# Kernel tuning notes

Measured on AMD Instinct MI355X. Metric: run time of the kernel, lower is better.

## Reference

```python
import jax, jax.numpy as jnp
import numpy as np
import math

D_MODEL = 1024
N_HEADS = 16
D_HEAD = 64


def setup_inputs() -> dict:
    key = jax.random.key(0)
    ks = jax.random.split(key, 9)
    B, T = 2, 2048
    s = 1.0 / math.sqrt(D_MODEL)
    return {
        "x": jax.random.normal(ks[0], (B, T, D_MODEL), dtype=jnp.float32),
        "Wq": jax.random.normal(ks[1], (D_MODEL, D_MODEL), dtype=jnp.float32) * s,
        "bq": jnp.zeros((D_MODEL,), dtype=jnp.float32),
        "Wk": jax.random.normal(ks[2], (D_MODEL, D_MODEL), dtype=jnp.float32) * s,
        "bk": jnp.zeros((D_MODEL,), dtype=jnp.float32),
        "Wv": jax.random.normal(ks[3], (D_MODEL, D_MODEL), dtype=jnp.float32) * s,
        "bv": jnp.zeros((D_MODEL,), dtype=jnp.float32),
        "Wo": jax.random.normal(ks[4], (D_MODEL, D_MODEL), dtype=jnp.float32) * s,
        "bo": jnp.zeros((D_MODEL,), dtype=jnp.float32),
    }


def reference(x, Wq, bq, Wk, bk, Wv, bv, Wo, bo):
    B, T, _ = x.shape
    # Linear layers (torch convention: y = x @ W^T + b)
    Q = x @ Wq.T + bq
    K = x @ Wk.T + bk
    V = x @ Wv.T + bv
    # [B, H, T, Dh]
    Q = Q.reshape(B, T, N_HEADS, D_HEAD).transpose(0, 2, 1, 3)
    K = K.reshape(B, T, N_HEADS, D_HEAD).transpose(0, 2, 1, 3)
    V = V.reshape(B, T, N_HEADS, D_HEAD).transpose(0, 2, 1, 3)
    scores = jnp.einsum("bhqd,bhkd->bhqk", Q, K) / math.sqrt(D_HEAD)
    causal_mask = jnp.tril(jnp.ones((T, T), dtype=bool))  # [T, T]
    scores = jnp.where(causal_mask, scores, -jnp.inf)
    attn = jax.nn.softmax(scores, axis=-1)
    out = jnp.einsum("bhqk,bhkd->bhqd", attn, V)
    out = out.transpose(0, 2, 1, 3).reshape(B, T, D_MODEL)
    return out @ Wo.T + bo
```

## Files before the change

### kernel.cpp

```cpp
#include <hip/hip_runtime.h>

typedef unsigned short u16;
typedef __bf16 bf16x8 __attribute__((ext_vector_type(8)));
typedef float f32x4 __attribute__((ext_vector_type(4)));
typedef float f32x16 __attribute__((ext_vector_type(16)));
typedef u16 u16x4 __attribute__((ext_vector_type(4)));
typedef unsigned int uint;

#define DM 1024
#define MROWS 4096
#define TSEQ 2048

static __device__ __forceinline__ u16 f2b(float f) {
  uint u = __builtin_bit_cast(uint, f);
  uint r = (u + 0x7fffu + ((u >> 16) & 1u)) >> 16;
  return (u16)r;
}

static __device__ __forceinline__ uint pkbf(float a, float b) {
  union { __bf16 h[2]; uint u; } x;
  x.h[0] = (__bf16)a; x.h[1] = (__bf16)b;
  return x.u;
}

__global__ __launch_bounds__(256) void cvt_kernel(const float* __restrict__ in,
                                                  u16* __restrict__ out, int n,
                                                  float scale) {
  int i = (blockIdx.x * 256 + threadIdx.x) * 4;
  if (i >= n) return;
  float4 v = *(const float4*)(in + i);
  u16x4 o;
  o.x = f2b(v.x * scale); o.y = f2b(v.y * scale);
  o.z = f2b(v.z * scale); o.w = f2b(v.w * scale);
  *(u16x4*)(out + i) = o;
}

__global__ __launch_bounds__(256) void cvt4_kernel(
    const float* __restrict__ w0, const float* __restrict__ w1,
    const float* __restrict__ w2, const float* __restrict__ w3,
    u16* __restrict__ o0, u16* __restrict__ o1, u16* __restrict__ o2,
    u16* __restrict__ o3, float s0) {
  const int sel = blockIdx.y;
  const float* in = (sel == 0) ? w0 : (sel == 1) ? w1 : (sel == 2) ? w2 : w3;
  u16* out = (sel == 0) ? o0 : (sel == 1) ? o1 : (sel == 2) ? o2 : o3;
  const float scale = (sel == 0) ? s0 : 1.0f;
  int i = (blockIdx.x * 256 + threadIdx.x) * 4;
  float4 v = *(const float4*)(in + i);
  u16x4 o;
  o.x = f2b(v.x * scale); o.y = f2b(v.y * scale);
  o.z = f2b(v.z * scale); o.w = f2b(v.w * scale);
  *(u16x4*)(out + i) = o;
}

#define SWZ(o) ((o) ^ ((((o) >> 7) & 3) << 4))

static __device__ __forceinline__ void gemm_tile(const u16* __restrict__ A,
                                                 const u16* __restrict__ W,
                                                 int row0, int col0,
                                                 char* ldsA, char* ldsB,
                                                 f32x4 (&acc)[4][4]) {
  const int tid = threadIdx.x;
  const int lane = tid & 63, wid = tid >> 6;
  const int wr = wid >> 1, wc = wid & 1;
  const int lg = lane >> 4, lr = lane & 15;

  f32x4 z = {0.f, 0.f, 0.f, 0.f};
#pragma unroll
  for (int m = 0; m < 4; ++m)
#pragma unroll
    for (int n = 0; n < 4; ++n) acc[m][n] = z;

  for (int k0 = 0; k0 < DM; k0 += 32) {
#pragma unroll
    for (int c = 0; c < 2; ++c) {
      int lin = (c * 256 + tid) * 16;
      int p = SWZ(lin);
      int rowl = p >> 6;
      int cb = p & 63;
      const char* ga = (const char*)(A + (size_t)(row0 + rowl) * DM + k0) + cb;
      __builtin_amdgcn_global_load_lds(
          (const __attribute__((address_space(1))) void*)ga,
          (__attribute__((address_space(3))) void*)(ldsA + lin), 16, 0, 0);
      const char* gb = (const char*)(W + (size_t)(col0 + rowl) * DM + k0) + cb;
      __builtin_amdgcn_global_load_lds(
          (const __attribute__((address_space(1))) void*)gb,
          (__attribute__((address_space(3))) void*)(ldsB + lin), 16, 0, 0);
    }
    __syncthreads();

    bf16x8 av[4], bv[4];
#pragma unroll
    for (int m = 0; m < 4; ++m) {
      int bo = (wr * 64 + m * 16 + lr) * 64 + lg * 16;
      av[m] = *(const bf16x8*)(ldsA + SWZ(bo));
    }
#pragma unroll
    for (int n = 0; n < 4; ++n) {
      int bo = (wc * 64 + n * 16 + lr) * 64 + lg * 16;
      bv[n] = *(const bf16x8*)(ldsB + SWZ(bo));
    }
#pragma unroll
    for (int m = 0; m < 4; ++m)
#pragma unroll
      for (int n = 0; n < 4; ++n)
        acc[m][n] = __builtin_amdgcn_mfma_f32_16x16x32_bf16(av[m], bv[n], acc[m][n], 0, 0, 0);
    __syncthreads();
  }
}

__global__ __launch_bounds__(256) void qkv_gemm(
    const u16* __restrict__ xb, const u16* __restrict__ Wqb,
    const u16* __restrict__ Wkb, const u16* __restrict__ Wvb,
    const float* __restrict__ bq, const float* __restrict__ bk,
    const float* __restrict__ bv, u16* __restrict__ Qx, u16* __restrict__ Kx,
    u16* __restrict__ Vx) {
  __shared__ char lds[16384];
  const int seg = blockIdx.x >> 3, nt = blockIdx.x & 7;
  const int row0 = blockIdx.y * 128, col0 = nt * 128;
  const u16* W = (seg == 0) ? Wqb : (seg == 1) ? Wkb : Wvb;
  const float* bias = (seg == 0) ? bq : (seg == 1) ? bk : bv;
  const float bscale = (seg == 0) ? 0.18033688011112042f : 1.0f;

  f32x4 acc[4][4];
  gemm_tile(xb, W, row0, col0, lds, lds + 8192, acc);

  const int tid = threadIdx.x;
  const int lane = tid & 63, wid = tid >> 6;
  const int wr = wid >> 1, wc = wid & 1;
  const int lg = lane >> 4, lr = lane & 15;

  if (seg < 2) {
    u16* out = (seg == 0) ? Qx : Kx;
#pragma unroll
    for (int m = 0; m < 4; ++m)
#pragma unroll
      for (int n = 0; n < 4; ++n) {
        int col = col0 + wc * 64 + n * 16 + lr;
        float b = bias[col] * bscale;
        int h = col >> 6, dh = col & 63;
        int c = dh >> 4, hi2 = (dh >> 3) & 1, j = dh & 7;
#pragma unroll
        for (int r = 0; r < 4; ++r) {
          int row = row0 + wr * 64 + m * 16 + lg * 4 + r;
          int bI = row >> 11, tt = row & 2047;
          int tw = tt >> 5, ln2 = tt & 31;
          size_t idx =
              ((((((size_t)(bI * 16 + h) * 64 + tw) * 4 + c) * 2 + hi2) * 32) +
               ln2) * 8 + j;
          out[idx] = f2b(acc[m][n][r] + b);
        }
      }
  } else {
#pragma unroll
    for (int m = 0; m < 4; ++m)
#pragma unroll
      for (int n = 0; n < 4; ++n) {
        int col = col0 + wc * 64 + n * 16 + lr;
        float b = bias[col];
        int h = col >> 6, d = col & 63;
        int hh = d >> 5, ln2 = d & 31;
        int t = row0 + wr * 64 + m * 16 + lg * 4;
        int bI = t >> 11, tt = t & 2047;
        int kt = tt >> 5, kvi = tt & 31;
        int c = kvi >> 4, rem = kvi & 15;
        int hi2 = (rem >> 2) & 1, jh = (rem >> 3) & 1;
        u16x4 pk;
        pk.x = f2b(acc[m][n][0] + b);
        pk.y = f2b(acc[m][n][1] + b);
        pk.z = f2b(acc[m][n][2] + b);
        pk.w = f2b(acc[m][n][3] + b);
        size_t idx =
            (((((((size_t)(bI * 16 + h) * 64 + kt) * 2 + c) * 2 + hh) * 2 +
               hi2) * 32) + ln2) * 8 + jh * 4;
        *(u16x4*)(Vx + idx) = pk;
      }
  }
}

__global__ __launch_bounds__(256, 4) void attn_kernel(const u16* __restrict__ Qx,
                                                      const u16* __restrict__ Kx,
                                                      const u16* __restrict__ Vx,
                                                      u16* __restrict__ Aout) {
  __shared__ float mrg[2][64][32];
  __shared__ float mml[2][32][2];
  const int tid = threadIdx.x, lane = tid & 63, wid = tid >> 6;
  const int hi = lane >> 5, ln = lane & 31;
  const int id = blockIdx.x + (blockIdx.y << 5);
  const int xcd = id & 7, idx = id >> 3;
  const int bh = xcd * 4 + (idx & 3);
  const int qt = 31 - (idx >> 2);
  const int b = bh >> 4, h = bh & 15;
  const int q0 = qt * 64 + (wid & 1) * 32;
  const int spl = wid >> 1;
  const int ntile = (q0 >> 5) + 1;
  const int half = (ntile + 1) >> 1;
  const int tbeg = spl ? half : 0;
  const int tend = spl ? ntile : half;

  const u16* Qp = Qx + ((size_t)bh * 64 + (q0 >> 5)) * 2048;
  const u16* Kbb = Kx + (size_t)bh * 64 * 2048;
  const u16* Vbb = Vx + (size_t)bh * 64 * 2048;

  bf16x8 qf[4];
#pragma unroll
  for (int c = 0; c < 4; ++c)
    qf[c] = *(const bf16x8*)(Qp + c * 512 + hi * 256 + ln * 8);

  f32x16 Oa, Ob;
#pragma unroll
  for (int r = 0; r < 16; ++r) { Oa[r] = 0.f; Ob[r] = 0.f; }
  float m = -1e30f, l = 0.f;

  bf16x8 kf[4], vf[4];
  auto loadK = [&](int kt) {
    const u16* Kp = Kbb + (size_t)kt * 2048;
#pragma unroll
    for (int c = 0; c < 4; ++c)
      kf[c] = *(const bf16x8*)(Kp + c * 512 + hi * 256 + ln * 8);
  };
  auto loadV = [&](int kt) {
    const u16* Vp = Vbb + (size_t)kt * 2048;
#pragma unroll
    for (int c = 0; c < 2; ++c)
#pragma unroll
      for (int hh = 0; hh < 2; ++hh)
        vf[2 * c + hh] =
            *(const bf16x8*)(Vp + (c * 2 + hh) * 512 + hi * 256 + ln * 8);
  };

  if (tbeg < tend) loadK(tbeg);
  for (int kt = tbeg; kt < tend; ++kt) {
    const int k0 = kt * 32;
    const bool diag = (kt == ntile - 1);
    loadV(kt);
    f32x16 S;
#pragma unroll
    for (int r = 0; r < 16; ++r) S[r] = 0.f;
    __builtin_amdgcn_s_setprio(1);
#pragma unroll
    for (int c = 0; c < 4; ++c)
      S = __builtin_amdgcn_mfma_f32_32x32x16_bf16(kf[c], qf[c], S, 0, 0, 0);
    __builtin_amdgcn_s_setprio(0);
    if (kt + 1 < tend) loadK(kt + 1);
    if (diag) {
      const int q = q0 + ln;
#pragma unroll
      for (int r = 0; r < 16; ++r) {
        int kv = k0 + (r & 3) + 8 * (r >> 2) + 4 * hi;
        if (kv > q) S[r] = -1e30f;
      }
    }
    float m0 = fmaxf(fmaxf(S[0], S[1]), fmaxf(S[2], S[3]));
    float m1 = fmaxf(fmaxf(S[4], S[5]), fmaxf(S[6], S[7]));
    float m2 = fmaxf(fmaxf(S[8], S[9]), fmaxf(S[10], S[11]));
    float m3 = fmaxf(fmaxf(S[12], S[13]), fmaxf(S[14], S[15]));
    float mx = fmaxf(fmaxf(m0, m1), fmaxf(m2, m3));
    mx = fmaxf(mx, __shfl_xor(mx, 32));
    if (!__all(mx - m <= 8.f)) {
      float nm = fmaxf(m, mx);
      float sf = __builtin_amdgcn_exp2f(m - nm);
      m = nm; l *= sf;
#pragma unroll
      for (int r = 0; r < 16; ++r) { Oa[r] *= sf; Ob[r] *= sf; }
    }
#pragma unroll
    for (int r = 0; r < 16; ++r) S[r] = __builtin_amdgcn_exp2f(S[r] - m);
    float ts = ((S[0] + S[1]) + (S[2] + S[3])) + ((S[4] + S[5]) + (S[6] + S[7]));
    ts += ((S[8] + S[9]) + (S[10] + S[11])) + ((S[12] + S[13]) + (S[14] + S[15]));
    ts += __shfl_xor(ts, 32);
    l += ts;
    uint pw[8];
#pragma unroll
    for (int i = 0; i < 8; ++i) pw[i] = pkbf(S[2 * i], S[2 * i + 1]);
    __builtin_amdgcn_s_setprio(1);
#pragma unroll
    for (int c = 0; c < 2; ++c) {
      union { uint w[4]; bf16x8 v; } pf;
      pf.w[0] = pw[4 * c + 0]; pf.w[1] = pw[4 * c + 1];
      pf.w[2] = pw[4 * c + 2]; pf.w[3] = pw[4 * c + 3];
      Oa = __builtin_amdgcn_mfma_f32_32x32x16_bf16(vf[2 * c + 0], pf.v, Oa, 0, 0, 0);
      Ob = __builtin_amdgcn_mfma_f32_32x32x16_bf16(vf[2 * c + 1], pf.v, Ob, 0, 0, 0);
    }
    __builtin_amdgcn_s_setprio(0);
  }

  union uo { f32x16 v; f32x4 q[4]; };
  const int pi = wid & 1;
  char* moc = (char*)&mrg[pi][0][0];
  const int sw8 = lane & 7;
  if (spl) {
    uo ua, ub; ua.v = Oa; ub.v = Ob;
#pragma unroll
    for (int c = 0; c < 4; ++c) {
      *(f32x4*)(moc + lane * 128 + ((c ^ sw8) * 16)) = ua.q[c];
      *(f32x4*)(moc + lane * 128 + (((c + 4) ^ sw8) * 16)) = ub.q[c];
    }
    if (hi == 0) { mml[pi][ln][0] = m; mml[pi][ln][1] = l; }
  }
  __syncthreads();
  if (spl) return;

  f32x4 rb[8];
#pragma unroll
  for (int c = 0; c < 8; ++c)
    rb[c] = *(const f32x4*)(moc + lane * 128 + ((c ^ sw8) * 16));
  float mB = mml[pi][ln][0], lB = mml[pi][ln][1];
  float M = fmaxf(m, mB);
  float eA = __builtin_amdgcn_exp2f(m - M);
  float eB = __builtin_amdgcn_exp2f(mB - M);
  float inv = 1.f / (l * eA + lB * eB);
  eA *= inv; eB *= inv;
  uo ua, ub; ua.v = Oa; ub.v = Ob;
#pragma unroll
  for (int c = 0; c < 4; ++c) {
    ua.q[c] = ua.q[c] * eA + rb[c] * eB;
    ub.q[c] = ub.q[c] * eA + rb[c + 4] * eB;
  }
  Oa = ua.v; Ob = ub.v;

  char* Tc = moc;
#pragma unroll
  for (int i = 0; i < 8; ++i) {
    int d0 = (2 * i & 3) + 8 * ((2 * i) >> 2) + 4 * hi;
    uint wA = pkbf(Oa[2 * i], Oa[2 * i + 1]);
    *(uint*)(Tc + (ln * 128 + ((d0 * 2) ^ ((ln & 7) << 4)))) = wA;
    uint wB = pkbf(Ob[2 * i], Ob[2 * i + 1]);
    *(uint*)(Tc + (ln * 128 + (((d0 + 32) * 2) ^ ((ln & 7) << 4)))) = wB;
  }
  __threadfence_block();
  u16* Ap = Aout + (size_t)b * TSEQ * DM + h * 64 + (size_t)(q0 + ln) * DM;
#pragma unroll
  for (int j = 0; j < 4; ++j) {
    int oct = hi * 4 + j;
    bf16x8 v = *(const bf16x8*)(Tc + (ln * 128 + ((oct * 16) ^ ((ln & 7) << 4))));
    *(bf16x8*)(Ap + oct * 8) = v;
  }
}

__global__ __launch_bounds__(256) void out_gemm(const u16* __restrict__ attn,
                                                const u16* __restrict__ Wob,
                                                const float* __restrict__ bo,
                                                float* __restrict__ out) {
  __shared__ char lds[16384];
  const int row0 = blockIdx.y * 128, col0 = blockIdx.x * 128;
  f32x4 acc[4][4];
  gemm_tile(attn, Wob, row0, col0, lds, lds + 8192, acc);

  const int tid = threadIdx.x;
  const int lane = tid & 63, wid = tid >> 6;
  const int wr = wid >> 1, wc = wid & 1;
  const int lg = lane >> 4, lr = lane & 15;
#pragma unroll
  for (int m = 0; m < 4; ++m)
#pragma unroll
    for (int n = 0; n < 4; ++n) {
      int col = col0 + wc * 64 + n * 16 + lr;
      float b = bo[col];
#pragma unroll
      for (int r = 0; r < 4; ++r) {
        int row = row0 + wr * 64 + m * 16 + lg * 4 + r;
        out[(size_t)row * DM + col] = acc[m][n][r] + b;
      }
    }
}

extern "C" void kernel_launch(void* const* d_in, const int* in_sizes, int n_in,
                              void* d_out, int out_size, void* d_ws, size_t ws_size,
                              hipStream_t stream) {
  const float* x = (const float*)d_in[0];
  const float* Wq = (const float*)d_in[1];
  const float* bq = (const float*)d_in[2];
  const float* Wk = (const float*)d_in[3];
  const float* bk = (const float*)d_in[4];
  const float* Wv = (const float*)d_in[5];
  const float* bv = (const float*)d_in[6];
  const float* Wo = (const float*)d_in[7];
  const float* bo = (const float*)d_in[8];

  char* ws = (char*)d_ws;
  const size_t MB = 1024 * 1024;
  u16* xb = (u16*)(ws);
  u16* Wqb = (u16*)(ws + 8 * MB);
  u16* Wkb = (u16*)(ws + 10 * MB);
  u16* Wvb = (u16*)(ws + 12 * MB);
  u16* Wob = (u16*)(ws + 14 * MB);
  u16* Qf = (u16*)(ws + 16 * MB);
  u16* Kf = (u16*)(ws + 24 * MB);
  u16* Vf = (u16*)(ws + 32 * MB);
  u16* attnb = xb;

  cvt_kernel<<<4096, 256, 0, stream>>>(x, xb, MROWS * DM, 1.0f);
  cvt4_kernel<<<dim3(1024, 4), 256, 0, stream>>>(Wq, Wk, Wv, Wo, Wqb, Wkb, Wvb,
                                                 Wob, 0.18033688011112042f);

  qkv_gemm<<<dim3(24, 32), 256, 0, stream>>>(xb, Wqb, Wkb, Wvb, bq, bk, bv, Qf, Kf, Vf);
  attn_kernel<<<dim3(32, 32), 256, 0, stream>>>(Qf, Kf, Vf, attnb);
  out_gemm<<<dim3(8, 32), 256, 0, stream>>>(attnb, Wob, bo, (float*)d_out);
}
```

Measured before the change: 113.5 us.

## Double-buffer GEMM LDS tiles and stage QKV epilogue through LDS for vector stores

```diff
diff --git a/kernel.cpp b/kernel.cpp
--- a/kernel.cpp
+++ b/kernel.cpp
@@ -57,54 +57,69 @@
 static __device__ __forceinline__ void gemm_tile(const u16* __restrict__ A,
                                                  const u16* __restrict__ W,
                                                  int row0, int col0,
-                                                 char* ldsA, char* ldsB,
+                                                 char* lds,
                                                  f32x4 (&acc)[4][4]) {
   const int tid = threadIdx.x;
   const int lane = tid & 63, wid = tid >> 6;
   const int wr = wid >> 1, wc = wid & 1;
   const int lg = lane >> 4, lr = lane & 15;
 
+  const u16* srcA[2]; const u16* srcB[2]; int dst[2];
+#pragma unroll
+  for (int c = 0; c < 2; ++c) {
+    int lin = (c * 256 + tid) * 16;
+    int p = SWZ(lin);
+    srcA[c] = A + (size_t)(row0 + (p >> 6)) * DM + ((p & 63) >> 1);
+    srcB[c] = W + (size_t)(col0 + (p >> 6)) * DM + ((p & 63) >> 1);
+    dst[c] = lin;
+  }
+  int offA[4], offB[4];
+#pragma unroll
+  for (int m = 0; m < 4; ++m) offA[m] = SWZ((wr * 64 + m * 16 + lr) * 64 + lg * 16);
+#pragma unroll
+  for (int n = 0; n < 4; ++n) offB[n] = SWZ((wc * 64 + n * 16 + lr) * 64 + lg * 16);
+
   f32x4 z = {0.f, 0.f, 0.f, 0.f};
 #pragma unroll
   for (int m = 0; m < 4; ++m)
 #pragma unroll
     for (int n = 0; n < 4; ++n) acc[m][n] = z;
 
+  auto stage = [&](int k0, int buf) {
+    char* bA = lds + buf * 16384;
+    char* bB = bA + 8192;
+#pragma unroll
+    for (int c = 0; c < 2; ++c) {
+      __builtin_amdgcn_global_load_lds(
+          (const __attribute__((address_space(1))) void*)(srcA[c] + k0),
+          (__attribute__((address_space(3))) void*)(bA + dst[c]), 16, 0, 0);
+      __builtin_amdgcn_global_load_lds(
+          (const __attribute__((address_space(1))) void*)(srcB[c] + k0),
+          (__attribute__((address_space(3))) void*)(bB + dst[c]), 16, 0, 0);
+    }
+  };
+
+  stage(0, 0);
+  __syncthreads();
+  int cur = 0;
   for (int k0 = 0; k0 < DM; k0 += 32) {
-#pragma unroll
-    for (int c = 0; c < 2; ++c) {
-      int lin = (c * 256 + tid) * 16;
-      int p = SWZ(lin);
-      int rowl = p >> 6;
-      int cb = p & 63;
-      const char* ga = (const char*)(A + (size_t)(row0 + rowl) * DM + k0) + cb;
-      __builtin_amdgcn_global_load_lds(
-          (const __attribute__((address_space(1))) void*)ga,
-          (__attribute__((address_space(3))) void*)(ldsA + lin), 16, 0, 0);
-      const char* gb = (const char*)(W + (size_t)(col0 + rowl) * DM + k0) + cb;
-      __builtin_amdgcn_global_load_lds(
-          (const __attribute__((address_space(1))) void*)gb,
-          (__attribute__((address_space(3))) void*)(ldsB + lin), 16, 0, 0);
-    }
-    __syncthreads();
-
+    if (k0 + 32 < DM) stage(k0 + 32, cur ^ 1);
+    char* bA = lds + cur * 16384;
+    char* bB = bA + 8192;
     bf16x8 av[4], bv[4];
 #pragma unroll
-    for (int m = 0; m < 4; ++m) {
-      int bo = (wr * 64 + m * 16 + lr) * 64 + lg * 16;
-      av[m] = *(const bf16x8*)(ldsA + SWZ(bo));
-    }
-#pragma unroll
-    for (int n = 0; n < 4; ++n) {
-      int bo = (wc * 64 + n * 16 + lr) * 64 + lg * 16;
-      bv[n] = *(const bf16x8*)(ldsB + SWZ(bo));
-    }
+    for (int m = 0; m < 4; ++m) av[m] = *(const bf16x8*)(bA + offA[m]);
+#pragma unroll
+    for (int n = 0; n < 4; ++n) bv[n] = *(const bf16x8*)(bB + offB[n]);
+    __builtin_amdgcn_s_setprio(1);
 #pragma unroll
     for (int m = 0; m < 4; ++m)
 #pragma unroll
       for (int n = 0; n < 4; ++n)
         acc[m][n] = __builtin_amdgcn_mfma_f32_16x16x32_bf16(av[m], bv[n], acc[m][n], 0, 0, 0);
+    __builtin_amdgcn_s_setprio(0);
     __syncthreads();
+    cur ^= 1;
   }
 }
 
@@ -114,7 +129,7 @@
     const float* __restrict__ bq, const float* __restrict__ bk,
     const float* __restrict__ bv, u16* __restrict__ Qx, u16* __restrict__ Kx,
     u16* __restrict__ Vx) {
-  __shared__ char lds[16384];
+  __shared__ char lds[32768];
   const int seg = blockIdx.x >> 3, nt = blockIdx.x & 7;
   const int row0 = blockIdx.y * 128, col0 = nt * 128;
   const u16* W = (seg == 0) ? Wqb : (seg == 1) ? Wkb : Wvb;
@@ -122,58 +137,66 @@
   const float bscale = (seg == 0) ? 0.18033688011112042f : 1.0f;
 
   f32x4 acc[4][4];
-  gemm_tile(xb, W, row0, col0, lds, lds + 8192, acc);
+  gemm_tile(xb, W, row0, col0, lds, acc);
 
   const int tid = threadIdx.x;
   const int lane = tid & 63, wid = tid >> 6;
   const int wr = wid >> 1, wc = wid & 1;
   const int lg = lane >> 4, lr = lane & 15;
 
+  float bcol[4];
+#pragma unroll
+  for (int n = 0; n < 4; ++n) bcol[n] = bias[col0 + wc * 64 + n * 16 + lr] * bscale;
+#pragma unroll
+  for (int m = 0; m < 4; ++m)
+#pragma unroll
+    for (int n = 0; n < 4; ++n) {
+      int colB = (wc * 64 + n * 16 + lr) * 2;
+#pragma unroll
+      for (int r = 0; r < 4; ++r) {
+        int row = wr * 64 + m * 16 + lg * 4 + r;
+        *(u16*)(lds + row * 256 + (colB ^ ((row & 7) << 4))) =
+            f2b(acc[m][n][r] + bcol[n]);
+      }
+    }
+  __syncthreads();
+
+  const int st = tid >> 5, lnq = tid & 31;
+  const int bI = row0 >> 11;
   if (seg < 2) {
     u16* out = (seg == 0) ? Qx : Kx;
-#pragma unroll
-    for (int m = 0; m < 4; ++m)
-#pragma unroll
-      for (int n = 0; n < 4; ++n) {
-        int col = col0 + wc * 64 + n * 16 + lr;
-        float b = bias[col] * bscale;
-        int h = col >> 6, dh = col & 63;
-        int c = dh >> 4, hi2 = (dh >> 3) & 1, j = dh & 7;
-#pragma unroll
-        for (int r = 0; r < 4; ++r) {
-          int row = row0 + wr * 64 + m * 16 + lg * 4 + r;
-          int bI = row >> 11, tt = row & 2047;
-          int tw = tt >> 5, ln2 = tt & 31;
-          size_t idx =
-              ((((((size_t)(bI * 16 + h) * 64 + tw) * 4 + c) * 2 + hi2) * 32) +
-               ln2) * 8 + j;
-          out[idx] = f2b(acc[m][n][r] + b);
-        }
+    const int hloc = st & 1, twloc = st >> 1;
+    const int h = (col0 >> 6) + hloc;
+    const int tw = ((row0 & 2047) >> 5) + twloc;
+    u16* base = out + ((size_t)(bI * 16 + h) * 64 + tw) * 2048;
+#pragma unroll
+    for (int ch = 0; ch < 8; ++ch) {
+      int q = ch * 256 + lnq * 8;
+      int c = q >> 9, hi2 = (q >> 8) & 1;
+      int row = twloc * 32 + lnq;
+      int colB = hloc * 128 + c * 32 + hi2 * 16;
+      bf16x8 v = *(const bf16x8*)(lds + row * 256 + (colB ^ ((row & 7) << 4)));
+      *(bf16x8*)(base + q) = v;
+    }
+  } else {
+    const int hloc = st & 1, ktloc = st >> 1;
+    const int h = (col0 >> 6) + hloc;
+    const int kt = ((row0 & 2047) >> 5) + ktloc;
+    u16* base = Vx + ((size_t)(bI * 16 + h) * 64 + kt) * 2048;
+#pragma unroll
+    for (int ch = 0; ch < 8; ++ch) {
+      int q = ch * 256 + lnq * 8;
+      int hi2 = ch & 1, hh = (ch >> 1) & 1, c = (ch >> 2) & 1;
+      int colB = (hloc * 64 + hh * 32 + lnq) * 2;
+      union { u16 a[8]; bf16x8 v; } t;
+#pragma unroll
+      for (int j = 0; j < 8; ++j) {
+        int kvi = 16 * c + (j & 3) + 8 * (j >> 2) + 4 * hi2;
+        int row = ktloc * 32 + kvi;
+        t.a[j] = *(const u16*)(lds + row * 256 + (colB ^ ((row & 7) << 4)));
       }
-  } else {
-#pragma unroll
-    for (int m = 0; m < 4; ++m)
-#pragma unroll
-      for (int n = 0; n < 4; ++n) {
-        int col = col0 + wc * 64 + n * 16 + lr;
-        float b = bias[col];
-        int h = col >> 6, d = col & 63;
-        int hh = d >> 5, ln2 = d & 31;
-        int t = row0 + wr * 64 + m * 16 + lg * 4;
-        int bI = t >> 11, tt = t & 2047;
-        int kt = tt >> 5, kvi = tt & 31;
-        int c = kvi >> 4, rem = kvi & 15;
-        int hi2 = (rem >> 2) & 1, jh = (rem >> 3) & 1;
-        u16x4 pk;
-        pk.x = f2b(acc[m][n][0] + b);
-        pk.y = f2b(acc[m][n][1] + b);
-        pk.z = f2b(acc[m][n][2] + b);
-        pk.w = f2b(acc[m][n][3] + b);
-        size_t idx =
-            (((((((size_t)(bI * 16 + h) * 64 + kt) * 2 + c) * 2 + hh) * 2 +
-               hi2) * 32) + ln2) * 8 + jh * 4;
-        *(u16x4*)(Vx + idx) = pk;
-      }
+      *(bf16x8*)(base + q) = t.v;
+    }
   }
 }
 
@@ -341,10 +364,10 @@
                                                 const u16* __restrict__ Wob,
                                                 const float* __restrict__ bo,
                                                 float* __restrict__ out) {
-  __shared__ char lds[16384];
+  __shared__ char lds[32768];
   const int row0 = blockIdx.y * 128, col0 = blockIdx.x * 128;
   f32x4 acc[4][4];
-  gemm_tile(attn, Wob, row0, col0, lds, lds + 8192, acc);
+  gemm_tile(attn, Wob, row0, col0, lds, acc);
 
   const int tid = threadIdx.x;
   const int lane = tid & 63, wid = tid >> 6;
```

After: 96.00 us. 1.18x faster.
